# Optimization experiments

Measured on AMD Instinct MI355X. Metric: run time of the kernel, lower is better.

Reference implementation:

```python
import jax, jax.numpy as jnp
import numpy as np

N_STREAMS = 4
N_HEADS = 4
D_STATE = 64
EPS_RMS = float(np.finfo(np.float32).eps)


def rms_norm(x, w):
    v = jnp.mean(x * x, axis=-1, keepdims=True)
    return x * jax.lax.rsqrt(v + EPS_RMS) * w


def sinkhorn_mix(logits, iters=5):
    n = logits.shape[0]
    M = jax.nn.sigmoid(logits) + jnp.eye(n, dtype=logits.dtype)
    for _ in range(iters):
        M = M / (M.sum(axis=1, keepdims=True) + 1e-6)
        M = M / (M.sum(axis=0, keepdims=True) + 1e-6)
    return M


def mamba_block(u, norm_w, Wi, bi, A_log, D, dt_bias, Wo, bo):
    B, L, d_model = u.shape
    d_in = 2 * d_model
    P = d_in // N_HEADS
    un = rms_norm(u, norm_w)
    zxbcdt = un @ Wi + bi  # [B,L,4612]
    z = zxbcdt[:, :, :d_in]
    x = zxbcdt[:, :, d_in:2 * d_in].reshape(B, L, N_HEADS, P)
    dt = zxbcdt[:, :, 2 * d_in:2 * d_in + N_HEADS]
    BC = zxbcdt[:, :, 2 * d_in + N_HEADS:].reshape(B, L, N_HEADS, 2, D_STATE)
    B_mat, C_mat = BC[:, :, :, 0], BC[:, :, :, 1]
    dt = jax.nn.softplus(dt + dt_bias)            # [B,L,H]
    A = -jnp.exp(A_log)                            # [H]
    dtA = jnp.exp(dt * A)                          # [B,L,H]
    dtB = dt[..., None] * B_mat                    # [B,L,H,N]

    # time-major scan over the selective-state recurrence
    def step(h, inp):
        dtA_t, dtB_t, x_t, C_t = inp               # [B,H],[B,H,N],[B,H,P],[B,H,N]
        h = h * dtA_t[:, :, None, None] + dtB_t[..., None] * x_t[:, :, None, :]
        y_t = jnp.einsum('bhn,bhnp->bhp', C_t, h)
        return h, y_t

    h0 = jnp.zeros((B, N_HEADS, D_STATE, P), dtype=u.dtype)
    xs = (jnp.moveaxis(dtA, 1, 0), jnp.moveaxis(dtB, 1, 0),
          jnp.moveaxis(x, 1, 0), jnp.moveaxis(C_mat, 1, 0))
    _, ys = jax.lax.scan(step, h0, xs)             # ys: [L,B,H,P]
    y = jnp.moveaxis(ys, 0, 1)                     # [B,L,H,P]
    y = y + x * D[None, None, :, None]
    y = y.reshape(B, L, d_in) * jax.nn.silu(z)
    return y @ Wo + bo


def setup_inputs() -> dict:
    key = jax.random.key(0)
    ks = jax.random.split(key, 10)
    B, L, d_model, vocab, n_layers = 2, 2048, 1024, 32000, 4
    d_proj_out = 2 * 2 * d_model + 2 * N_HEADS * D_STATE + N_HEADS  # 4612
    d_in = 2 * d_model
    s = lambda f: 1.0 / np.sqrt(f)
    return {
        'tokens': jax.random.randint(ks[0], (B, L), 0, vocab, dtype=jnp.int32),
        'embed': jax.random.normal(ks[1], (vocab, d_model), jnp.float32) * 0.02,
        'norm_w': jnp.ones((n_layers, d_model), jnp.float32),
        'in_proj_W': jax.random.normal(ks[2], (n_layers, d_model, d_proj_out), jnp.float32) * s(d_model),
        'in_proj_b': jnp.zeros((n_layers, d_proj_out), jnp.float32),
        'A_log': jnp.full((n_layers, N_HEADS), -4.0, jnp.float32),
        'D': jnp.ones((n_layers, N_HEADS), jnp.float32),
        'dt_bias': jax.random.uniform(ks[3], (n_layers, N_HEADS), jnp.float32) - 4.0,
        'out_proj_W': jax.random.normal(ks[4], (n_layers, d_in, d_model), jnp.float32) * s(d_in),
        'out_proj_b': jnp.zeros((n_layers, d_model), jnp.float32),
        'mixer_logits': jax.random.normal(ks[5], (n_layers, N_STREAMS, N_STREAMS), jnp.float32) * 0.1,
        'norm_f_w': jnp.ones((d_model,), jnp.float32),
        'head_W': jax.random.normal(ks[6], (d_model, vocab), jnp.float32) * s(d_model),
        'head_b': jnp.zeros((vocab,), jnp.float32),
    }


def reference(tokens, embed, norm_w, in_proj_W, in_proj_b, A_log, D, dt_bias,
              out_proj_W, out_proj_b, mixer_logits, norm_f_w, head_W, head_b):
    B, L = tokens.shape
    d_model = embed.shape[1]
    d_sub = d_model // N_STREAMS
    x = embed[tokens]                              # [B,L,d_model]
    H = x.reshape(B, L, N_STREAMS, d_sub)
    n_layers = norm_w.shape[0]
    for l in range(n_layers):
        M = sinkhorn_mix(mixer_logits[l])
        H_res = jnp.einsum('bsid,ji->bsjd', H, M)
        x_out = mamba_block(H.reshape(B, L, d_model), norm_w[l], in_proj_W[l],
                            in_proj_b[l], A_log[l], D[l], dt_bias[l],
                            out_proj_W[l], out_proj_b[l])
        H = H_res + x_out.reshape(B, L, N_STREAMS, d_sub)
    out = rms_norm(H.reshape(B, L, d_model), norm_f_w)
    return out @ head_W + head_b
```

## Files before the change

kernel.cpp:

```cpp
#include <hip/hip_runtime.h>
#include <hip/hip_fp16.h>
#include <cstdint>


typedef _Float16 f16;
typedef __attribute__((ext_vector_type(8))) _Float16 f16x8;
typedef __attribute__((ext_vector_type(4))) _Float16 f16x4;
typedef __attribute__((ext_vector_type(4))) float f32x4;

#define LDS_CAST(p) ((__attribute__((address_space(3))) void*)(p))
#define GLB_CAST(p) ((const __attribute__((address_space(1))) void*)(p))

static __device__ __forceinline__ void gload16(const void* g, void* l) {
    __builtin_amdgcn_global_load_lds(GLB_CAST(g), LDS_CAST(l), 16, 0, 0);
}

__global__ __launch_bounds__(512, 2) void gemm256(
    const f16* __restrict__ A, const f16* __restrict__ Bt,
    const float* __restrict__ bias, float* __restrict__ C,
    int M, int N, int K)
{
    __shared__ f16 AS[4 * 256 * 32];
    __shared__ f16 BS[4 * 256 * 32];

    const int tid = threadIdx.x;
    const int lane = tid & 63;
    const int w = tid >> 6;
    const int wr = w >> 2;
    const int wc = w & 3;
    const int mrow = lane & 15, ksel = lane >> 4;

    const int gx = gridDim.x;
    const int gy = gridDim.y;
    const int nwg = gx * gy;
    int lin = blockIdx.y * gx + blockIdx.x;
    int xcd = lin & 7, loc = lin >> 3;
    int q = nwg >> 3, rr = nwg & 7;
    int wg = (xcd < rr) ? (xcd * (q + 1) + loc)
                        : (rr * (q + 1) + (xcd - rr) * q + loc);
    const int GROUP = 8;
    int per_group = GROUP * gy;
    int gid = wg / per_group;
    int first_m = gid * GROUP;
    int gsz = (gx - first_m < GROUP) ? (gx - first_m) : GROUP;
    int inner = wg - gid * per_group;
    const int m0 = (first_m + inner % gsz) * 256;
    const int n0 = (inner / gsz) * 256;

    const int rowt = tid >> 2;
    const int colE = ((tid & 3) ^ ((rowt >> 1) & 3)) * 8;
    const int ldst = tid * 8;

    const f16* gA = A + (size_t)m0 * K;
    const f16* gB = Bt + (size_t)n0 * K;
    const size_t gofsA0 = (size_t)rowt * K + colE;
    const size_t gofsA1 = (size_t)(128 + rowt) * K + colE;
    const size_t gofsB0 = gofsA0;
    const size_t gofsB1 = gofsA1;

    const int fcol = ((ksel ^ ((mrow >> 1) & 3)) * 8);
    int offA[8], offB[4];
#pragma unroll
    for (int mf = 0; mf < 8; mf++)
        offA[mf] = (wr * 128 + mf * 16 + mrow) * 32 + fcol;
#pragma unroll
    for (int nf = 0; nf < 4; nf++)
        offB[nf] = (wc * 64 + nf * 16 + mrow) * 32 + fcol;

    f32x4 zero = {0.f, 0.f, 0.f, 0.f};
    f32x4 acc[8][4];
#pragma unroll
    for (int i = 0; i < 8; i++)
#pragma unroll
        for (int j = 0; j < 4; j++) acc[i][j] = zero;

    const int nt = K >> 5;

#pragma unroll
    for (int T = 0; T < 3; ++T) {
        gload16(gA + gofsA0 + (size_t)T * 32, AS + T * 8192 + ldst);
        gload16(gA + gofsA1 + (size_t)T * 32, AS + T * 8192 + 4096 + ldst);
        gload16(gB + gofsB0 + (size_t)T * 32, BS + T * 8192 + ldst);
        gload16(gB + gofsB1 + (size_t)T * 32, BS + T * 8192 + 4096 + ldst);
    }
    asm volatile("s_waitcnt vmcnt(8)" ::: "memory");
    __builtin_amdgcn_sched_barrier(0);
    __builtin_amdgcn_s_barrier();

    for (int t = 0; t < nt; ++t) {
        const int slot = t & 3;
        const f16* as = AS + slot * 8192;
        const f16* bs = BS + slot * 8192;
        const int sst = (t + 3) & 3;
        const bool st = (t + 3) < nt;
        const size_t kof = (size_t)(t + 3) * 32;

        f16x8 af[4], bf[4];
#pragma unroll
        for (int mf = 0; mf < 4; mf++) af[mf] = *(const f16x8*)(as + offA[mf]);
#pragma unroll
        for (int nf = 0; nf < 4; nf++) bf[nf] = *(const f16x8*)(bs + offB[nf]);
        if (st) {
            gload16(gA + gofsA0 + kof, AS + sst * 8192 + ldst);
            gload16(gA + gofsA1 + kof, AS + sst * 8192 + 4096 + ldst);
        }
        __builtin_amdgcn_s_barrier();
        __builtin_amdgcn_s_setprio(1);
#pragma unroll
        for (int mf = 0; mf < 4; mf++)
#pragma unroll
            for (int nf = 0; nf < 4; nf++)
                acc[mf][nf] = __builtin_amdgcn_mfma_f32_16x16x32_f16(bf[nf], af[mf], acc[mf][nf], 0, 0, 0);
        __builtin_amdgcn_s_setprio(0);
        __builtin_amdgcn_s_barrier();

        f16x8 af2[4];
#pragma unroll
        for (int mf = 0; mf < 4; mf++) af2[mf] = *(const f16x8*)(as + offA[4 + mf]);
        if (st) {
            gload16(gB + gofsB0 + kof, BS + sst * 8192 + ldst);
            gload16(gB + gofsB1 + kof, BS + sst * 8192 + 4096 + ldst);
        }
        __builtin_amdgcn_s_barrier();
        __builtin_amdgcn_s_setprio(1);
#pragma unroll
        for (int mf = 0; mf < 4; mf++)
#pragma unroll
            for (int nf = 0; nf < 4; nf++)
                acc[4 + mf][nf] = __builtin_amdgcn_mfma_f32_16x16x32_f16(bf[nf], af2[mf], acc[4 + mf][nf], 0, 0, 0);
        __builtin_amdgcn_s_setprio(0);

        if (t + 1 < nt) {
            const int rem = nt - t - 2;
            if (rem >= 2) {
                asm volatile("s_waitcnt vmcnt(8)" ::: "memory");
            } else if (rem == 1) {
                asm volatile("s_waitcnt vmcnt(4)" ::: "memory");
            } else {
                asm volatile("s_waitcnt vmcnt(0)" ::: "memory");
            }
            __builtin_amdgcn_sched_barrier(0);
            __builtin_amdgcn_s_barrier();
        }
    }

#pragma unroll
    for (int mf = 0; mf < 8; mf++) {
        int m = m0 + wr * 128 + mf * 16 + mrow;
#pragma unroll
        for (int nf = 0; nf < 4; nf++) {
            int nb = n0 + wc * 64 + nf * 16 + ksel * 4;
            if (nb < N) {
                float4 bv = {0.f, 0.f, 0.f, 0.f};
                if (bias) bv = *(const float4*)(bias + nb);
                float4 v;
                v.x = acc[mf][nf][0] + bv.x;
                v.y = acc[mf][nf][1] + bv.y;
                v.z = acc[mf][nf][2] + bv.z;
                v.w = acc[mf][nf][3] + bv.w;
                *(float4*)(C + (size_t)m * N + nb) = v;
            }
        }
    }
}

__global__ __launch_bounds__(256) void gemm_f16(
    const f16* __restrict__ A, const f16* __restrict__ Bt,
    const float* __restrict__ bias, float* __restrict__ C,
    int M, int N, int K)
{
    __shared__ f16 As[128 * 32];
    __shared__ f16 Bs[128 * 32];
    const int t = threadIdx.x;
    const int lane = t & 63;
    const int w = t >> 6;

    const int gx = gridDim.x;
    const int gy = gridDim.y;
    const int nwg = gx * gy;
    int lin = blockIdx.y * gx + blockIdx.x;
    int xcd = lin & 7, loc = lin >> 3;
    int q = nwg >> 3, rr = nwg & 7;
    int wg = (xcd < rr) ? (xcd * (q + 1) + loc)
                        : (rr * (q + 1) + (xcd - rr) * q + loc);
    const int GROUP = 8;
    int per_group = GROUP * gy;
    int gid = wg / per_group;
    int first_m = gid * GROUP;
    int gsz = (gx - first_m < GROUP) ? (gx - first_m) : GROUP;
    int inner = wg - gid * per_group;
    const int m0 = (first_m + inner % gsz) * 128;
    const int n0 = (inner / gsz) * 128;

    const int wm0 = (w >> 1) * 64, wn0 = (w & 1) * 64;
    const int mrow = lane & 15, ksel = lane >> 4;

    f32x4 zero = {0.f, 0.f, 0.f, 0.f};
    f32x4 acc[4][4];
#pragma unroll
    for (int i = 0; i < 4; i++)
#pragma unroll
        for (int j = 0; j < 4; j++) acc[i][j] = zero;

    const f16* Abase = A + (size_t)m0 * K;
    const f16* Bbase = Bt + (size_t)n0 * K;

    for (int k0 = 0; k0 < K; k0 += 32) {
#pragma unroll
        for (int i = 0; i < 2; i++) {
            int lin2 = t + i * 256;
            int r = lin2 >> 2;
            int cc = (lin2 & 3) * 8;
            gload16(Abase + (size_t)r * K + k0 + cc, As + lin2 * 8);
            gload16(Bbase + (size_t)r * K + k0 + cc, Bs + lin2 * 8);
        }
        __syncthreads();
        f16x8 af[4], bf[4];
#pragma unroll
        for (int i = 0; i < 4; i++) {
            af[i] = *(const f16x8*)(As + (wm0 + i * 16 + mrow) * 32 + ksel * 8);
            bf[i] = *(const f16x8*)(Bs + (wn0 + i * 16 + mrow) * 32 + ksel * 8);
        }
#pragma unroll
        for (int i = 0; i < 4; i++)
#pragma unroll
            for (int j = 0; j < 4; j++)
                acc[i][j] = __builtin_amdgcn_mfma_f32_16x16x32_f16(bf[j], af[i], acc[i][j], 0, 0, 0);
        __syncthreads();
    }

#pragma unroll
    for (int i = 0; i < 4; i++) {
        int m = m0 + wm0 + i * 16 + mrow;
#pragma unroll
        for (int j = 0; j < 4; j++) {
            int nb = n0 + wn0 + j * 16 + ksel * 4;
            if (nb < N) {
                float4 bv = {0.f, 0.f, 0.f, 0.f};
                if (bias) bv = *(const float4*)(bias + nb);
                float4 v;
                v.x = acc[i][j][0] + bv.x;
                v.y = acc[i][j][1] + bv.y;
                v.z = acc[i][j][2] + bv.z;
                v.w = acc[i][j][3] + bv.w;
                *(float4*)(C + (size_t)m * N + nb) = v;
            }
        }
    }
}

__global__ __launch_bounds__(256) void transpose_w(
    const float* __restrict__ W, f16* __restrict__ Wt, int K, int N, int Npad)
{
    __shared__ float tile[32][33];
    int n0 = blockIdx.x * 32, k0 = blockIdx.y * 32;
    int tx = threadIdx.x & 31, ty = threadIdx.x >> 5;
#pragma unroll
    for (int i = 0; i < 4; i++) {
        int k = k0 + ty + 8 * i;
        int n = n0 + tx;
        tile[ty + 8 * i][tx] = (n < N) ? W[(size_t)k * N + n] : 0.f;
    }
    __syncthreads();
#pragma unroll
    for (int i = 0; i < 4; i++) {
        int n = n0 + ty + 8 * i;
        if (n < Npad) Wt[(size_t)n * K + k0 + tx] = (f16)tile[tx][ty + 8 * i];
    }
}

__global__ void sinkhorn_k(const float* __restrict__ logits, float* __restrict__ Mout)
{
    if (threadIdx.x != 0 || blockIdx.x != 0) return;
    for (int l = 0; l < 4; l++) {
        float M[16];
        for (int i = 0; i < 16; i++) {
            float v = logits[l * 16 + i];
            M[i] = 1.f / (1.f + __expf(-v)) + ((i % 5) == 0 ? 1.f : 0.f);
        }
        for (int it = 0; it < 5; it++) {
            for (int r = 0; r < 4; r++) {
                float s = M[r*4] + M[r*4+1] + M[r*4+2] + M[r*4+3] + 1e-6f;
                for (int c = 0; c < 4; c++) M[r*4+c] /= s;
            }
            for (int c = 0; c < 4; c++) {
                float s = M[c] + M[4+c] + M[8+c] + M[12+c] + 1e-6f;
                for (int r = 0; r < 4; r++) M[r*4+c] /= s;
            }
        }
        for (int i = 0; i < 16; i++) Mout[l * 16 + i] = M[i];
    }
}

__global__ __launch_bounds__(256) void embed_gather(
    const int* __restrict__ tokens, const float* __restrict__ embed, float* __restrict__ H)
{
    int i = blockIdx.x * 256 + threadIdx.x;
    int tok = i >> 8, d4 = i & 255;
    int tk = tokens[tok];
    float4 v = ((const float4*)(embed + (size_t)tk * 1024))[d4];
    ((float4*)(H + (size_t)tok * 1024))[d4] = v;
}

__global__ __launch_bounds__(256) void rmsnorm_k(
    const float* __restrict__ X, const float* __restrict__ w, f16* __restrict__ out)
{
    int tok = blockIdx.x;
    int t = threadIdx.x;
    const float4 v = ((const float4*)(X + (size_t)tok * 1024))[t];
    float ss = v.x*v.x + v.y*v.y + v.z*v.z + v.w*v.w;
#pragma unroll
    for (int off = 32; off > 0; off >>= 1) ss += __shfl_down(ss, off, 64);
    __shared__ float wsum[4];
    if ((t & 63) == 0) wsum[t >> 6] = ss;
    __syncthreads();
    float tot = wsum[0] + wsum[1] + wsum[2] + wsum[3];
    float sc = rsqrtf(tot * (1.f / 1024.f) + 1.1920929e-07f);
    const float4 wv = ((const float4*)w)[t];
    f16x4 o;
    o[0] = (f16)(v.x * sc * wv.x);
    o[1] = (f16)(v.y * sc * wv.y);
    o[2] = (f16)(v.z * sc * wv.z);
    o[3] = (f16)(v.w * sc * wv.w);
    ((f16x4*)(out + (size_t)tok * 1024))[t] = o;
}

__global__ __launch_bounds__(256) void dt_cumsum(
    const float* __restrict__ zx, const float* __restrict__ dt_bias,
    const float* __restrict__ A_log,
    float* __restrict__ dt, float* __restrict__ cum, float* __restrict__ E)
{
    int bh = blockIdx.x;
    int b = bh >> 2, h = bh & 3;
    int t = threadIdx.x;
    float Ah = -__expf(A_log[h]);
    float bias = dt_bias[h];
    float run = 0.f, vals[8];
    for (int i = 0; i < 8; i++) {
        int l = t * 8 + i;
        float raw = zx[((size_t)(b * 2048 + l)) * 4612 + 4096 + h] + bias;
        float dtv = (raw > 20.f) ? raw : log1pf(__expf(raw));
        dt[bh * 2048 + l] = dtv;
        run += dtv * Ah;
        vals[i] = run;
    }
    __shared__ float ps[256];
    ps[t] = run;
    __syncthreads();
    for (int off = 1; off < 256; off <<= 1) {
        float v = (t >= off) ? ps[t - off] : 0.f;
        __syncthreads();
        ps[t] += v;
        __syncthreads();
    }
    float offset = (t > 0) ? ps[t - 1] : 0.f;
    for (int i = 0; i < 8; i++) {
        int l = t * 8 + i;
        float cv = vals[i] + offset;
        cum[bh * 2048 + l] = cv;
        if ((l & 63) == 63) E[bh * 32 + (l >> 6)] = cv;
    }
}

__global__ __launch_bounds__(256) void make_xT(
    const float* __restrict__ zx, f16* __restrict__ xT)
{
    int lb = blockIdx.x * 64, pb = blockIdx.y * 64, bh = blockIdx.z;
    int b = bh >> 2, h = bh & 3;
    __shared__ float tile[64][65];
    int tx = threadIdx.x & 63, ty = threadIdx.x >> 6;
#pragma unroll
    for (int i = 0; i < 16; i++) {
        int ll = ty + 4 * i;
        tile[ll][tx] = zx[((size_t)(b * 2048 + lb + ll)) * 4612 + 2048 + h * 512 + pb + tx];
    }
    __syncthreads();
#pragma unroll
    for (int i = 0; i < 16; i++) {
        int pl = ty + 4 * i;
        xT[((size_t)bh * 512 + pb + pl) * 2048 + lb + tx] = (f16)tile[tx][pl];
    }
}

__global__ __launch_bounds__(256) void make_BC(
    const float* __restrict__ zx, f16* __restrict__ Bc, f16* __restrict__ Cc)
{
    int i = blockIdx.x * 256 + threadIdx.x;
    int n = i & 63, h = (i >> 6) & 3, l = (i >> 8) & 2047, b = i >> 19;
    size_t rowoff = ((size_t)(b * 2048 + l)) * 4612 + 4100 + h * 128;
    size_t o = (((size_t)(b * 4 + h)) * 2048 + l) * 64 + n;
    Bc[o] = (f16)zx[rowoff + n];
    Cc[o] = (f16)zx[rowoff + 64 + n];
}

__global__ __launch_bounds__(256) void chunk_intra(
    const f16* __restrict__ Bc, const f16* __restrict__ Cc,
    const f16* __restrict__ xT,
    const float* __restrict__ dt, const float* __restrict__ cum,
    float* __restrict__ Y, float* __restrict__ Hloc)
{
    int c = blockIdx.x, bh = blockIdx.y;
    int l0 = c * 64;
    __shared__ f16 Cs[4096], Bs2[4096], Sb[4096], Wb[4096];
    __shared__ float cums[64], dts[64];
    int t = threadIdx.x;
    {
        const f16x8* sC = (const f16x8*)(Cc + ((size_t)bh * 2048 + l0) * 64);
        const f16x8* sB = (const f16x8*)(Bc + ((size_t)bh * 2048 + l0) * 64);
        ((f16x8*)Cs)[t] = sC[t];
        ((f16x8*)Cs)[t + 256] = sC[t + 256];
        ((f16x8*)Bs2)[t] = sB[t];
        ((f16x8*)Bs2)[t + 256] = sB[t + 256];
    }
    if (t < 64) {
        cums[t] = cum[bh * 2048 + l0 + t];
        dts[t] = dt[bh * 2048 + l0 + t];
    }
    __syncthreads();
    float cumEnd = cums[63];
    int lane = t & 63, w = t >> 6;
    int mrow = lane & 15, ksel = lane >> 4;

    {
        f16x8 cf[2];
        cf[0] = *(const f16x8*)(Cs + (w * 16 + mrow) * 64 + ksel * 8);
        cf[1] = *(const f16x8*)(Cs + (w * 16 + mrow) * 64 + 32 + ksel * 8);
#pragma unroll
        for (int j = 0; j < 4; j++) {
            f32x4 d = {0.f, 0.f, 0.f, 0.f};
#pragma unroll
            for (int ks = 0; ks < 2; ks++) {
                f16x8 bfv = *(const f16x8*)(Bs2 + (j * 16 + mrow) * 64 + ks * 32 + ksel * 8);
                d = __builtin_amdgcn_mfma_f32_16x16x32_f16(cf[ks], bfv, d, 0, 0, 0);
            }
            int ss = j * 16 + mrow;
#pragma unroll
            for (int r = 0; r < 4; r++) {
                int tt = w * 16 + ksel * 4 + r;
                float sv = (ss <= tt) ? d[r] * __expf(cums[tt] - cums[ss]) * dts[ss] : 0.f;
                Sb[tt * 64 + ss] = (f16)sv;
            }
        }
#pragma unroll
        for (int q2 = 0; q2 < 16; q2++) {
            int idx = t * 16 + q2;
            int tt = idx >> 6, ss = idx & 63;
            float wv = (float)Bs2[ss * 64 + tt] * __expf(cumEnd - cums[ss]) * dts[ss];
            Wb[tt * 64 + ss] = (f16)wv;
        }
    }
    __syncthreads();

    f16x8 sfr[2][4], wfr[2][4];
#pragma unroll
    for (int ks = 0; ks < 2; ks++)
#pragma unroll
        for (int mt = 0; mt < 4; mt++) {
            sfr[ks][mt] = *(const f16x8*)(Sb + (mt * 16 + mrow) * 64 + ks * 32 + ksel * 8);
            wfr[ks][mt] = *(const f16x8*)(Wb + (mt * 16 + mrow) * 64 + ks * 32 + ksel * 8);
        }
    const f16* xbase = xT + ((size_t)bh * 512) * 2048 + c * 64;
    f32x4 zero = {0.f, 0.f, 0.f, 0.f};
#pragma unroll
    for (int ph = 0; ph < 2; ph++) {
        int pb = w * 128 + ph * 64;
        f32x4 aY[4][4], aH[4][4];
#pragma unroll
        for (int i = 0; i < 4; i++)
#pragma unroll
            for (int j = 0; j < 4; j++) { aY[i][j] = zero; aH[i][j] = zero; }
#pragma unroll
        for (int ks = 0; ks < 2; ks++) {
#pragma unroll
            for (int nt = 0; nt < 4; nt++) {
                int pp = pb + nt * 16 + mrow;
                f16x8 bfv = *(const f16x8*)(xbase + (size_t)pp * 2048 + ks * 32 + ksel * 8);
#pragma unroll
                for (int mt = 0; mt < 4; mt++) {
                    aY[mt][nt] = __builtin_amdgcn_mfma_f32_16x16x32_f16(sfr[ks][mt], bfv, aY[mt][nt], 0, 0, 0);
                    aH[mt][nt] = __builtin_amdgcn_mfma_f32_16x16x32_f16(wfr[ks][mt], bfv, aH[mt][nt], 0, 0, 0);
                }
            }
        }
        int r0 = ksel * 4;
#pragma unroll
        for (int mt = 0; mt < 4; mt++)
#pragma unroll
            for (int nt = 0; nt < 4; nt++) {
                int pp = pb + nt * 16 + mrow;
#pragma unroll
                for (int r = 0; r < 4; r++) {
                    int tt = mt * 16 + r0 + r;
                    Y[((size_t)bh * 2048 + l0 + tt) * 512 + pp] = aY[mt][nt][r];
                    Hloc[(((size_t)bh * 32 + c) * 64 + tt) * 512 + pp] = aH[mt][nt][r];
                }
            }
    }
}

__global__ __launch_bounds__(256) void chunk_scan(
    const float* __restrict__ Hloc, const float* __restrict__ E,
    f16* __restrict__ HpreT)
{
    int bh = blockIdx.y;
    int p = blockIdx.x * 64 + (threadIdx.x & 63);
    int nb = blockIdx.z * 16 + (threadIdx.x >> 6) * 4;
    float h[4];
#pragma unroll
    for (int j = 0; j < 4; j++) h[j] = 0.f;
    float Eprev = 0.f;
    for (int c = 0; c < 32; c++) {
        size_t ob = (((size_t)bh * 32 + c) * 512 + p) * 64 + nb;
        f16x4 v;
#pragma unroll
        for (int j = 0; j < 4; j++) v[j] = (f16)h[j];
        *(f16x4*)(HpreT + ob) = v;
        float Ec = E[bh * 32 + c];
        float decay = __expf(Ec - Eprev);
        Eprev = Ec;
        size_t ib = (((size_t)bh * 32 + c) * 64 + nb) * 512 + p;
#pragma unroll
        for (int j = 0; j < 4; j++)
            h[j] = decay * h[j] + Hloc[ib + (size_t)j * 512];
    }
}

__global__ __launch_bounds__(256) void chunk_inter(
    const f16* __restrict__ Cc, const f16* __restrict__ HpreT,
    const float* __restrict__ cum, const float* __restrict__ E,
    const float* __restrict__ Y, const float* __restrict__ zx,
    const float* __restrict__ Dp, f16* __restrict__ ybuf)
{
    int c = blockIdx.x, bh = blockIdx.y;
    int b = bh >> 2, h = bh & 3;
    int l0 = c * 64;
    __shared__ f16 Chat[4096];
    int t = threadIdx.x;
    float Eprev = (c > 0) ? E[bh * 32 + c - 1] : 0.f;
    for (int i = t; i < 4096; i += 256) {
        int tt = i >> 6, n = i & 63;
        float cv = (float)Cc[((size_t)bh * 2048 + l0 + tt) * 64 + n];
        Chat[i] = (f16)(cv * __expf(cum[bh * 2048 + l0 + tt] - Eprev));
    }
    __syncthreads();
    int lane = t & 63, w = t >> 6;
    int mrow = lane & 15, ksel = lane >> 4;
    float Dh = Dp[h];
    f16x8 af[2][4];
#pragma unroll
    for (int ks = 0; ks < 2; ks++)
#pragma unroll
        for (int mt = 0; mt < 4; mt++)
            af[ks][mt] = *(const f16x8*)(Chat + (mt * 16 + mrow) * 64 + ks * 32 + ksel * 8);
    const f16* hb = HpreT + (((size_t)bh * 32 + c) * 512) * 64;
    f32x4 zero = {0.f, 0.f, 0.f, 0.f};
#pragma unroll
    for (int ph = 0; ph < 2; ph++) {
        int pb = w * 128 + ph * 64;
        f32x4 acc[4][4];
#pragma unroll
        for (int i = 0; i < 4; i++)
#pragma unroll
            for (int j = 0; j < 4; j++) acc[i][j] = zero;
#pragma unroll
        for (int ks = 0; ks < 2; ks++) {
#pragma unroll
            for (int nt = 0; nt < 4; nt++) {
                int pp = pb + nt * 16 + mrow;
                f16x8 bfv = *(const f16x8*)(hb + (size_t)pp * 64 + ks * 32 + ksel * 8);
#pragma unroll
                for (int mt = 0; mt < 4; mt++)
                    acc[mt][nt] = __builtin_amdgcn_mfma_f32_16x16x32_f16(af[ks][mt], bfv, acc[mt][nt], 0, 0, 0);
            }
        }
        int r0 = ksel * 4;
#pragma unroll
        for (int mt = 0; mt < 4; mt++)
#pragma unroll
            for (int nt = 0; nt < 4; nt++) {
                int pp = pb + nt * 16 + mrow;
#pragma unroll
                for (int r = 0; r < 4; r++) {
                    int tt = mt * 16 + r0 + r;
                    int l = l0 + tt;
                    size_t zrow = ((size_t)(b * 2048 + l)) * 4612;
                    float y = acc[mt][nt][r] + Y[((size_t)bh * 2048 + l) * 512 + pp];
                    float x = zx[zrow + 2048 + h * 512 + pp];
                    y += x * Dh;
                    float z = zx[zrow + h * 512 + pp];
                    float sig = 1.f / (1.f + __expf(-z));
                    ybuf[((size_t)(b * 2048 + l)) * 2048 + h * 512 + pp] = (f16)(y * z * sig);
                }
            }
    }
}

__global__ __launch_bounds__(256) void mix_add(
    const float* __restrict__ Hold, const float* __restrict__ xout,
    const float* __restrict__ Mm, float* __restrict__ Hnew)
{
    int i = blockIdx.x * 256 + threadIdx.x;
    int j = i & 255, tok = i >> 8;
    size_t rb = (size_t)tok * 1024;
    float h0 = Hold[rb + j], h1 = Hold[rb + 256 + j];
    float h2 = Hold[rb + 512 + j], h3 = Hold[rb + 768 + j];
#pragma unroll
    for (int s = 0; s < 4; s++) {
        float v = Mm[s*4+0]*h0 + Mm[s*4+1]*h1 + Mm[s*4+2]*h2 + Mm[s*4+3]*h3
                + xout[rb + s * 256 + j];
        Hnew[rb + s * 256 + j] = v;
    }
}

extern "C" void kernel_launch(void* const* d_in, const int* in_sizes, int n_in,
                              void* d_out, int out_size, void* d_ws, size_t ws_size,
                              hipStream_t stream)
{
    const int*   tokens     = (const int*)d_in[0];
    const float* embed      = (const float*)d_in[1];
    const float* norm_w     = (const float*)d_in[2];
    const float* in_proj_W  = (const float*)d_in[3];
    const float* in_proj_b  = (const float*)d_in[4];
    const float* A_log      = (const float*)d_in[5];
    const float* Dp         = (const float*)d_in[6];
    const float* dt_bias    = (const float*)d_in[7];
    const float* out_proj_W = (const float*)d_in[8];
    const float* out_proj_b = (const float*)d_in[9];
    const float* mixer_log  = (const float*)d_in[10];
    const float* norm_f_w   = (const float*)d_in[11];
    const float* head_W     = (const float*)d_in[12];
    const float* head_b     = (const float*)d_in[13];
    float* out = (float*)d_out;
    (void)in_sizes; (void)n_in; (void)out_size; (void)ws_size;

    char* base = (char*)d_ws;
    size_t off = 0;
    auto alloc = [&](size_t bytes) -> void* {
        void* r = (void*)(base + off);
        off = (off + bytes + 255) & ~(size_t)255;
        return r;
    };
    f16*   WinT   = (f16*)alloc(4ull * 4864 * 1024 * 2);
    f16*   WoutT  = (f16*)alloc(4ull * 1024 * 2048 * 2);
    f16*   WheadT = (f16*)alloc(32000ull * 1024 * 2);
    float* Mall   = (float*)alloc(64 * 4);
    float* H0     = (float*)alloc(4096ull * 1024 * 4);
    float* H1     = (float*)alloc(4096ull * 1024 * 4);
    f16*   un     = (f16*)alloc(4096ull * 1024 * 2);
    float* zx     = (float*)alloc(4096ull * 4612 * 4);
    float* dtb    = (float*)alloc(8ull * 2048 * 4);
    float* cumb   = (float*)alloc(8ull * 2048 * 4);
    float* Eb     = (float*)alloc(8ull * 32 * 4);
    f16*   xT     = (f16*)alloc(8ull * 512 * 2048 * 2);
    f16*   Bc     = (f16*)alloc(8ull * 2048 * 64 * 2);
    f16*   Cc     = (f16*)alloc(8ull * 2048 * 64 * 2);
    float* Yb     = (float*)alloc(8ull * 2048 * 512 * 4);
    float* Hloc   = (float*)alloc(8ull * 32 * 64 * 512 * 4);
    f16*   HpreT  = (f16*)alloc(8ull * 32 * 512 * 64 * 2);
    f16*   ybuf   = (f16*)alloc(4096ull * 2048 * 2);
    float* xout   = (float*)alloc(4096ull * 1024 * 4);

    for (int l = 0; l < 4; l++) {
        transpose_w<<<dim3(152, 32), 256, 0, stream>>>(
            in_proj_W + (size_t)l * 1024 * 4612, WinT + (size_t)l * 4864 * 1024,
            1024, 4612, 4864);
        transpose_w<<<dim3(32, 64), 256, 0, stream>>>(
            out_proj_W + (size_t)l * 2048 * 1024, WoutT + (size_t)l * 1024 * 2048,
            2048, 1024, 1024);
    }
    transpose_w<<<dim3(1000, 32), 256, 0, stream>>>(head_W, WheadT, 1024, 32000, 32000);
    sinkhorn_k<<<1, 64, 0, stream>>>(mixer_log, Mall);
    embed_gather<<<4096, 256, 0, stream>>>(tokens, embed, H0);

    float* Hc = H0;
    float* Hn = H1;
    for (int l = 0; l < 4; l++) {
        rmsnorm_k<<<4096, 256, 0, stream>>>(Hc, norm_w + l * 1024, un);
        gemm256<<<dim3(16, 19), 512, 0, stream>>>(
            un, WinT + (size_t)l * 4864 * 1024, in_proj_b + l * 4612, zx,
            4096, 4612, 1024);
        dt_cumsum<<<8, 256, 0, stream>>>(zx, dt_bias + l * 4, A_log + l * 4, dtb, cumb, Eb);
        make_xT<<<dim3(32, 8, 8), 256, 0, stream>>>(zx, xT);
        make_BC<<<4096, 256, 0, stream>>>(zx, Bc, Cc);
        chunk_intra<<<dim3(32, 8), 256, 0, stream>>>(Bc, Cc, xT, dtb, cumb, Yb, Hloc);
        chunk_scan<<<dim3(8, 8, 4), 256, 0, stream>>>(Hloc, Eb, HpreT);
        chunk_inter<<<dim3(32, 8), 256, 0, stream>>>(Cc, HpreT, cumb, Eb, Yb, zx, Dp + l * 4, ybuf);
        gemm_f16<<<dim3(32, 8), 256, 0, stream>>>(
            ybuf, WoutT + (size_t)l * 1024 * 2048, out_proj_b + l * 1024, xout,
            4096, 1024, 2048);
        mix_add<<<4096, 256, 0, stream>>>(Hc, xout, Mall + l * 16, Hn);
        float* tmp = Hc; Hc = Hn; Hn = tmp;
    }
    rmsnorm_k<<<4096, 256, 0, stream>>>(Hc, norm_f_w, un);
    gemm256<<<dim3(16, 125), 512, 0, stream>>>(un, WheadT, head_b, out, 4096, 32000, 1024);
}
```

Before: 2.065 ms.

## Move intra-chunk Y computation into chunk_inter and store Hloc in fp16

The intra-chunk diagonal output (S·x) is no longer computed in chunk_intra and written to a float32 Y buffer. chunk_inter now builds S itself and accumulates S·x and Ĉ·Hpre into the same accumulator, so the fp32 Y write and read-back disappear. chunk_intraH only computes the chunk-local state, which is now stored in fp16, halving Hloc traffic. In exchange chunk_inter loads B, C and x again and does more per-block work, and the chunk states lose some precision.

```diff
diff --git a/kernel.cpp b/kernel.cpp
--- a/kernel.cpp
+++ b/kernel.cpp
@@ -393,15 +393,119 @@
     Cc[o] = (f16)zx[rowoff + 64 + n];
 }
 
-__global__ __launch_bounds__(256) void chunk_intra(
-    const f16* __restrict__ Bc, const f16* __restrict__ Cc,
-    const f16* __restrict__ xT,
+__global__ __launch_bounds__(256) void chunk_intraH(
+    const f16* __restrict__ Bc, const f16* __restrict__ xT,
     const float* __restrict__ dt, const float* __restrict__ cum,
-    float* __restrict__ Y, float* __restrict__ Hloc)
+    f16* __restrict__ Hloc)
 {
     int c = blockIdx.x, bh = blockIdx.y;
     int l0 = c * 64;
-    __shared__ f16 Cs[4096], Bs2[4096], Sb[4096], Wb[4096];
+    __shared__ f16 Bs2[4096], Wb[4096];
+    __shared__ float cums[64], dts[64];
+    int t = threadIdx.x;
+    {
+        const f16x8* sB = (const f16x8*)(Bc + ((size_t)bh * 2048 + l0) * 64);
+        ((f16x8*)Bs2)[t] = sB[t];
+        ((f16x8*)Bs2)[t + 256] = sB[t + 256];
+    }
+    if (t < 64) {
+        cums[t] = cum[bh * 2048 + l0 + t];
+        dts[t] = dt[bh * 2048 + l0 + t];
+    }
+    __syncthreads();
+    float cumEnd = cums[63];
+    int lane = t & 63, w = t >> 6;
+    int mrow = lane & 15, ksel = lane >> 4;
+
+#pragma unroll
+    for (int q2 = 0; q2 < 16; q2++) {
+        int idx = t * 16 + q2;
+        int tt = idx >> 6, ss = idx & 63;
+        float wv = (float)Bs2[ss * 64 + tt] * __expf(cumEnd - cums[ss]) * dts[ss];
+        Wb[tt * 64 + ss] = (f16)wv;
+    }
+    __syncthreads();
+
+    f16x8 wfr[2][4];
+#pragma unroll
+    for (int ks = 0; ks < 2; ks++)
+#pragma unroll
+        for (int mt = 0; mt < 4; mt++)
+            wfr[ks][mt] = *(const f16x8*)(Wb + (mt * 16 + mrow) * 64 + ks * 32 + ksel * 8);
+    const f16* xbase = xT + ((size_t)bh * 512) * 2048 + c * 64;
+    f32x4 zero = {0.f, 0.f, 0.f, 0.f};
+#pragma unroll
+    for (int ph = 0; ph < 2; ph++) {
+        int pb = w * 128 + ph * 64;
+        f32x4 aH[4][4];
+#pragma unroll
+        for (int i = 0; i < 4; i++)
+#pragma unroll
+            for (int j = 0; j < 4; j++) aH[i][j] = zero;
+#pragma unroll
+        for (int ks = 0; ks < 2; ks++) {
+#pragma unroll
+            for (int nt = 0; nt < 4; nt++) {
+                int pp = pb + nt * 16 + mrow;
+                f16x8 bfv = *(const f16x8*)(xbase + (size_t)pp * 2048 + ks * 32 + ksel * 8);
+#pragma unroll
+                for (int mt = 0; mt < 4; mt++)
+                    aH[mt][nt] = __builtin_amdgcn_mfma_f32_16x16x32_f16(wfr[ks][mt], bfv, aH[mt][nt], 0, 0, 0);
+            }
+        }
+        int r0 = ksel * 4;
+#pragma unroll
+        for (int mt = 0; mt < 4; mt++)
+#pragma unroll
+            for (int nt = 0; nt < 4; nt++) {
+                int pp = pb + nt * 16 + mrow;
+#pragma unroll
+                for (int r = 0; r < 4; r++) {
+                    int tt = mt * 16 + r0 + r;
+                    Hloc[(((size_t)bh * 32 + c) * 64 + tt) * 512 + pp] = (f16)aH[mt][nt][r];
+                }
+            }
+    }
+}
+
+__global__ __launch_bounds__(256) void chunk_scan(
+    const f16* __restrict__ Hloc, const float* __restrict__ E,
+    f16* __restrict__ HpreT)
+{
+    int bh = blockIdx.y;
+    int p = blockIdx.x * 64 + (threadIdx.x & 63);
+    int nb = blockIdx.z * 16 + (threadIdx.x >> 6) * 4;
+    float h[4];
+#pragma unroll
+    for (int j = 0; j < 4; j++) h[j] = 0.f;
+    float Eprev = 0.f;
+    for (int c = 0; c < 32; c++) {
+        size_t ob = (((size_t)bh * 32 + c) * 512 + p) * 64 + nb;
+        f16x4 v;
+#pragma unroll
+        for (int j = 0; j < 4; j++) v[j] = (f16)h[j];
+        *(f16x4*)(HpreT + ob) = v;
+        float Ec = E[bh * 32 + c];
+        float decay = __expf(Ec - Eprev);
+        Eprev = Ec;
+        size_t ib = (((size_t)bh * 32 + c) * 64 + nb) * 512 + p;
+#pragma unroll
+        for (int j = 0; j < 4; j++)
+            h[j] = decay * h[j] + (float)Hloc[ib + (size_t)j * 512];
+    }
+}
+
+__global__ __launch_bounds__(256) void chunk_inter(
+    const f16* __restrict__ Bc, const f16* __restrict__ Cc,
+    const f16* __restrict__ HpreT, const f16* __restrict__ xT,
+    const float* __restrict__ dt, const float* __restrict__ cum,
+    const float* __restrict__ E, const float* __restrict__ zx,
+    const float* __restrict__ Dp, f16* __restrict__ ybuf)
+{
+    int c = blockIdx.x, bh = blockIdx.y;
+    int b = bh >> 2, h = bh & 3;
+    int l0 = c * 64;
+    __shared__ f16 Cs[4096], Bs2[4096], Sb[4096], Chat[4096];
     __shared__ float cums[64], dts[64];
     int t = threadIdx.x;
     {
@@ -417,10 +521,14 @@
         dts[t] = dt[bh * 2048 + l0 + t];
     }
     __syncthreads();
-    float cumEnd = cums[63];
     int lane = t & 63, w = t >> 6;
     int mrow = lane & 15, ksel = lane >> 4;
-
+    float Eprev = (c > 0) ? E[bh * 32 + c - 1] : 0.f;
+
+    for (int i = t; i < 4096; i += 256) {
+        int tt = i >> 6;
+        Chat[i] = (f16)((float)Cs[i] * __expf(cums[tt] - Eprev));
+    }
     {
         f16x8 cf[2];
         cf[0] = *(const f16x8*)(Cs + (w * 16 + mrow) * 64 + ksel * 8);
@@ -441,118 +549,20 @@
                 Sb[tt * 64 + ss] = (f16)sv;
             }
         }
-#pragma unroll
-        for (int q2 = 0; q2 < 16; q2++) {
-            int idx = t * 16 + q2;
-            int tt = idx >> 6, ss = idx & 63;
-            float wv = (float)Bs2[ss * 64 + tt] * __expf(cumEnd - cums[ss]) * dts[ss];
-            Wb[tt * 64 + ss] = (f16)wv;
-        }
     }
     __syncthreads();
 
-    f16x8 sfr[2][4], wfr[2][4];
+    f16x8 sfr[2][4], cfr[2][4];
 #pragma unroll
     for (int ks = 0; ks < 2; ks++)
 #pragma unroll
         for (int mt = 0; mt < 4; mt++) {
             sfr[ks][mt] = *(const f16x8*)(Sb + (mt * 16 + mrow) * 64 + ks * 32 + ksel * 8);
-            wfr[ks][mt] = *(const f16x8*)(Wb + (mt * 16 + mrow) * 64 + ks * 32 + ksel * 8);
+            cfr[ks][mt] = *(const f16x8*)(Chat + (mt * 16 + mrow) * 64 + ks * 32 + ksel * 8);
         }
     const f16* xbase = xT + ((size_t)bh * 512) * 2048 + c * 64;
-    f32x4 zero = {0.f, 0.f, 0.f, 0.f};
-#pragma unroll
-    for (int ph = 0; ph < 2; ph++) {
-        int pb = w * 128 + ph * 64;
-        f32x4 aY[4][4], aH[4][4];
-#pragma unroll
-        for (int i = 0; i < 4; i++)
-#pragma unroll
-            for (int j = 0; j < 4; j++) { aY[i][j] = zero; aH[i][j] = zero; }
-#pragma unroll
-        for (int ks = 0; ks < 2; ks++) {
-#pragma unroll
-            for (int nt = 0; nt < 4; nt++) {
-                int pp = pb + nt * 16 + mrow;
-                f16x8 bfv = *(const f16x8*)(xbase + (size_t)pp * 2048 + ks * 32 + ksel * 8);
-#pragma unroll
-                for (int mt = 0; mt < 4; mt++) {
-                    aY[mt][nt] = __builtin_amdgcn_mfma_f32_16x16x32_f16(sfr[ks][mt], bfv, aY[mt][nt], 0, 0, 0);
-                    aH[mt][nt] = __builtin_amdgcn_mfma_f32_16x16x32_f16(wfr[ks][mt], bfv, aH[mt][nt], 0, 0, 0);
-                }
-            }
-        }
-        int r0 = ksel * 4;
-#pragma unroll
-        for (int mt = 0; mt < 4; mt++)
-#pragma unroll
-            for (int nt = 0; nt < 4; nt++) {
-                int pp = pb + nt * 16 + mrow;
-#pragma unroll
-                for (int r = 0; r < 4; r++) {
-                    int tt = mt * 16 + r0 + r;
-                    Y[((size_t)bh * 2048 + l0 + tt) * 512 + pp] = aY[mt][nt][r];
-                    Hloc[(((size_t)bh * 32 + c) * 64 + tt) * 512 + pp] = aH[mt][nt][r];
-                }
-            }
-    }
-}
-
-__global__ __launch_bounds__(256) void chunk_scan(
-    const float* __restrict__ Hloc, const float* __restrict__ E,
-    f16* __restrict__ HpreT)
-{
-    int bh = blockIdx.y;
-    int p = blockIdx.x * 64 + (threadIdx.x & 63);
-    int nb = blockIdx.z * 16 + (threadIdx.x >> 6) * 4;
-    float h[4];
-#pragma unroll
-    for (int j = 0; j < 4; j++) h[j] = 0.f;
-    float Eprev = 0.f;
-    for (int c = 0; c < 32; c++) {
-        size_t ob = (((size_t)bh * 32 + c) * 512 + p) * 64 + nb;
-        f16x4 v;
-#pragma unroll
-        for (int j = 0; j < 4; j++) v[j] = (f16)h[j];
-        *(f16x4*)(HpreT + ob) = v;
-        float Ec = E[bh * 32 + c];
-        float decay = __expf(Ec - Eprev);
-        Eprev = Ec;
-        size_t ib = (((size_t)bh * 32 + c) * 64 + nb) * 512 + p;
-#pragma unroll
-        for (int j = 0; j < 4; j++)
-            h[j] = decay * h[j] + Hloc[ib + (size_t)j * 512];
-    }
-}
-
-__global__ __launch_bounds__(256) void chunk_inter(
-    const f16* __restrict__ Cc, const f16* __restrict__ HpreT,
-    const float* __restrict__ cum, const float* __restrict__ E,
-    const float* __restrict__ Y, const float* __restrict__ zx,
-    const float* __restrict__ Dp, f16* __restrict__ ybuf)
-{
-    int c = blockIdx.x, bh = blockIdx.y;
-    int b = bh >> 2, h = bh & 3;
-    int l0 = c * 64;
-    __shared__ f16 Chat[4096];
-    int t = threadIdx.x;
-    float Eprev = (c > 0) ? E[bh * 32 + c - 1] : 0.f;
-    for (int i = t; i < 4096; i += 256) {
-        int tt = i >> 6, n = i & 63;
-        float cv = (float)Cc[((size_t)bh * 2048 + l0 + tt) * 64 + n];
-        Chat[i] = (f16)(cv * __expf(cum[bh * 2048 + l0 + tt] - Eprev));
-    }
-    __syncthreads();
-    int lane = t & 63, w = t >> 6;
-    int mrow = lane & 15, ksel = lane >> 4;
+    const f16* hb = HpreT + (((size_t)bh * 32 + c) * 512) * 64;
     float Dh = Dp[h];
-    f16x8 af[2][4];
-#pragma unroll
-    for (int ks = 0; ks < 2; ks++)
-#pragma unroll
-        for (int mt = 0; mt < 4; mt++)
-            af[ks][mt] = *(const f16x8*)(Chat + (mt * 16 + mrow) * 64 + ks * 32 + ksel * 8);
-    const f16* hb = HpreT + (((size_t)bh * 32 + c) * 512) * 64;
     f32x4 zero = {0.f, 0.f, 0.f, 0.f};
 #pragma unroll
     for (int ph = 0; ph < 2; ph++) {
@@ -567,10 +577,13 @@
 #pragma unroll
             for (int nt = 0; nt < 4; nt++) {
                 int pp = pb + nt * 16 + mrow;
-                f16x8 bfv = *(const f16x8*)(hb + (size_t)pp * 64 + ks * 32 + ksel * 8);
-#pragma unroll
-                for (int mt = 0; mt < 4; mt++)
-                    acc[mt][nt] = __builtin_amdgcn_mfma_f32_16x16x32_f16(af[ks][mt], bfv, acc[mt][nt], 0, 0, 0);
+                f16x8 xfv = *(const f16x8*)(xbase + (size_t)pp * 2048 + ks * 32 + ksel * 8);
+                f16x8 hfv = *(const f16x8*)(hb + (size_t)pp * 64 + ks * 32 + ksel * 8);
+#pragma unroll
+                for (int mt = 0; mt < 4; mt++) {
+                    acc[mt][nt] = __builtin_amdgcn_mfma_f32_16x16x32_f16(sfr[ks][mt], xfv, acc[mt][nt], 0, 0, 0);
+                    acc[mt][nt] = __builtin_amdgcn_mfma_f32_16x16x32_f16(cfr[ks][mt], hfv, acc[mt][nt], 0, 0, 0);
+                }
             }
         }
         int r0 = ksel * 4;
@@ -584,7 +597,7 @@
                     int tt = mt * 16 + r0 + r;
                     int l = l0 + tt;
                     size_t zrow = ((size_t)(b * 2048 + l)) * 4612;
-                    float y = acc[mt][nt][r] + Y[((size_t)bh * 2048 + l) * 512 + pp];
+                    float y = acc[mt][nt][r];
                     float x = zx[zrow + 2048 + h * 512 + pp];
                     y += x * Dh;
                     float z = zx[zrow + h * 512 + pp];
@@ -654,8 +667,7 @@
     f16*   xT     = (f16*)alloc(8ull * 512 * 2048 * 2);
     f16*   Bc     = (f16*)alloc(8ull * 2048 * 64 * 2);
     f16*   Cc     = (f16*)alloc(8ull * 2048 * 64 * 2);
-    float* Yb     = (float*)alloc(8ull * 2048 * 512 * 4);
-    float* Hloc   = (float*)alloc(8ull * 32 * 64 * 512 * 4);
+    f16*   Hloc   = (f16*)alloc(8ull * 32 * 64 * 512 * 2);
     f16*   HpreT  = (f16*)alloc(8ull * 32 * 512 * 64 * 2);
     f16*   ybuf   = (f16*)alloc(4096ull * 2048 * 2);
     float* xout   = (float*)alloc(4096ull * 1024 * 4);
@@ -682,9 +694,10 @@
         dt_cumsum<<<8, 256, 0, stream>>>(zx, dt_bias + l * 4, A_log + l * 4, dtb, cumb, Eb);
         make_xT<<<dim3(32, 8, 8), 256, 0, stream>>>(zx, xT);
         make_BC<<<4096, 256, 0, stream>>>(zx, Bc, Cc);
-        chunk_intra<<<dim3(32, 8), 256, 0, stream>>>(Bc, Cc, xT, dtb, cumb, Yb, Hloc);
+        chunk_intraH<<<dim3(32, 8), 256, 0, stream>>>(Bc, xT, dtb, cumb, Hloc);
         chunk_scan<<<dim3(8, 8, 4), 256, 0, stream>>>(Hloc, Eb, HpreT);
-        chunk_inter<<<dim3(32, 8), 256, 0, stream>>>(Cc, HpreT, cumb, Eb, Yb, zx, Dp + l * 4, ybuf);
+        chunk_inter<<<dim3(32, 8), 256, 0, stream>>>(
+            Bc, Cc, HpreT, xT, dtb, cumb, Eb, zx, Dp + l * 4, ybuf);
         gemm_f16<<<dim3(32, 8), 256, 0, stream>>>(
             ybuf, WoutT + (size_t)l * 1024 * 2048, out_proj_b + l * 1024, xout,
             4096, 1024, 2048);
```

Result: slower. 2.197 ms (+6.4%).
